# Performance work log

Hardware: AMD Instinct MI355X
Metric: run time of the kernel (lower is better)

Reference implementation:

```python
import jax, jax.numpy as jnp
import numpy as np

B, N, C, H = 4, 2048, 1024, 16
D = C // H  # head_dim = 64

def setup_inputs() -> dict:
    key = jax.random.key(0)
    k1, k2, k3, k4, k5, k6 = jax.random.split(key, 6)
    x = jax.random.normal(k1, (B, N, C), dtype=jnp.float32)
    rope_cos = jax.random.uniform(k2, (N, D), dtype=jnp.float32)
    rope_sin = jax.random.uniform(k3, (N, D), dtype=jnp.float32)
    w_qkv = jax.random.normal(k4, (3 * C, C), dtype=jnp.float32) * (C ** -0.5)
    w_proj = jax.random.normal(k5, (C, C), dtype=jnp.float32) * (C ** -0.5)
    b_proj = jax.random.normal(k6, (C,), dtype=jnp.float32) * 0.01
    return {"x": x, "rope_cos": rope_cos, "rope_sin": rope_sin,
            "w_qkv": w_qkv, "w_proj": w_proj, "b_proj": b_proj}

def _rotate_half(x):
    x1, x2 = jnp.split(x, 2, axis=-1)
    return jnp.concatenate((-x2, x1), axis=-1)

def _apply_rope(x, cos, sin):
    # x: [B,H,N,D]; cos/sin: [N,D] broadcast over B,H
    return x * cos + _rotate_half(x) * sin

def reference(x, rope_cos, rope_sin, w_qkv, w_proj, b_proj):
    Bc, Nc, Cc = x.shape
    scale = D ** -0.5
    qkv = jnp.einsum('bnc,fc->bnf', x, w_qkv)            # [B,N,3C]
    qkv = qkv.reshape(Bc, Nc, 3, H, D).transpose(2, 0, 3, 1, 4)  # [3,B,H,N,D]
    q, k, v = qkv[0], qkv[1], qkv[2]
    q = _apply_rope(q, rope_cos, rope_sin)
    k = _apply_rope(k, rope_cos, rope_sin)
    attn = jnp.einsum('bhnd,bhmd->bhnm', q, k) * scale   # [B,H,N,N]
    attn = jax.nn.softmax(attn, axis=-1)
    out = jnp.einsum('bhnm,bhmd->bhnd', attn, v)         # [B,H,N,D]
    out = out.transpose(0, 2, 1, 3).reshape(Bc, Nc, Cc)  # [B,N,C]
    return jnp.einsum('bnc,fc->bnf', out, w_proj) + b_proj
```

## Files before the change

kernel.cpp:

```cpp
#include <hip/hip_runtime.h>

#define MM   8192
#define CC   1024
#define F3   3072
#define NN   2048
#define HH   16
#define DD   64
#define QSCALE 0.1803368801111731f

typedef __attribute__((ext_vector_type(8))) __bf16 bf16x8;
typedef __attribute__((ext_vector_type(4))) float floatx4;
typedef __attribute__((ext_vector_type(4))) unsigned uintx4;

__device__ __forceinline__ unsigned short f2b(float f) {
  union { float f; unsigned int u; } v; v.f = f;
  unsigned int r = v.u + 0x7fffu + ((v.u >> 16) & 1u);
  return (unsigned short)(r >> 16);
}
__device__ __forceinline__ float b2f(unsigned short b) {
  union { unsigned int u; float f; } v; v.u = ((unsigned int)b) << 16;
  return v.f;
}

__device__ __forceinline__ void gl_lds16(const unsigned short* g, unsigned short* l) {
  __builtin_amdgcn_global_load_lds((const __attribute__((address_space(1))) void*)g,
                                   (__attribute__((address_space(3))) void*)l, 16, 0, 0);
}

__global__ __launch_bounds__(256) void cvt_all_k(const float* __restrict__ x,
                                                 const float* __restrict__ wqkv,
                                                 const float* __restrict__ wproj,
                                                 unsigned short* __restrict__ xb,
                                                 unsigned short* __restrict__ wqkvb,
                                                 unsigned short* __restrict__ wprojb) {
  const int N0 = MM * CC / 4, N1 = F3 * CC / 4, N2 = CC * CC / 4;
  const int total = N0 + N1 + N2;
  const int stride = (int)gridDim.x * 256;
  for (int i = blockIdx.x * 256 + threadIdx.x; i < total; i += stride) {
    const float* src;
    unsigned short* dst;
    int j;
    if (i < N0)            { src = x;     dst = xb;     j = i; }
    else if (i < N0 + N1)  { src = wqkv;  dst = wqkvb;  j = i - N0; }
    else                   { src = wproj; dst = wprojb; j = i - N0 - N1; }
    float4 v = ((const float4*)src)[j];
    ushort4 o;
    o.x = f2b(v.x); o.y = f2b(v.y); o.z = f2b(v.z); o.w = f2b(v.w);
    ((ushort4*)dst)[j] = o;
  }
}

template <int F, bool BF16OUT, bool ROPE>
__global__ __launch_bounds__(512, 2) void gemm_p(const unsigned short* __restrict__ A,
                                                 const unsigned short* __restrict__ Bm,
                                                 void* __restrict__ Cout,
                                                 const float* __restrict__ bias,
                                                 const float* __restrict__ rcp,
                                                 const float* __restrict__ spp, int K) {
  __shared__ alignas(16) unsigned short lA[3][128 * 64];
  __shared__ alignas(16) unsigned short lB[3][256 * 64];
  const int tid = threadIdx.x, lane = tid & 63, wave = tid >> 6;
  const int r16 = lane & 15, q4 = lane >> 4;
  const int wm = wave & 1, wn = wave >> 1;

  const int id = blockIdx.x;
  const int xcd = id & 7, slot = id >> 3;
  const int rx = xcd * 8 + (slot & 7), cy = slot >> 3;
  const int rowBase = rx * 128, colBase = cy * 256;

  const int cA0 = tid, cA1 = tid + 512;
  const int cB0 = tid, cB1 = tid + 512, cB2 = tid + 1024, cB3 = tid + 1536;
#define CHOFF(base, c) ((size_t)((base) + ((c) >> 3)) * K + ((((c) & 7) ^ (((c) >> 3) & 7)) << 3))
  const size_t aoff0 = CHOFF(rowBase, cA0), aoff1 = CHOFF(rowBase, cA1);
  const size_t boff0 = CHOFF(colBase, cB0), boff1 = CHOFF(colBase, cB1);
  const size_t boff2 = CHOFF(colBase, cB2), boff3 = CHOFF(colBase, cB3);
#undef CHOFF

#define STAGEP(kt, bsel) do { const int _k0 = (kt) * 64; \
    gl_lds16(A + aoff0 + _k0, &lA[bsel][cA0 * 8]); \
    gl_lds16(A + aoff1 + _k0, &lA[bsel][cA1 * 8]); \
    gl_lds16(Bm + boff0 + _k0, &lB[bsel][cB0 * 8]); \
    gl_lds16(Bm + boff1 + _k0, &lB[bsel][cB1 * 8]); \
    gl_lds16(Bm + boff2 + _k0, &lB[bsel][cB2 * 8]); \
    gl_lds16(Bm + boff3 + _k0, &lB[bsel][cB3 * 8]); } while (0)

  floatx4 acc[4][4];
  const floatx4 z = {0.f, 0.f, 0.f, 0.f};
#pragma unroll
  for (int i = 0; i < 4; ++i)
#pragma unroll
    for (int j = 0; j < 4; ++j) acc[i][j] = z;

  const int nt = K / 64;

  STAGEP(0, 0);
  STAGEP(1, 1);
  STAGEP(2, 2);
  asm volatile("s_waitcnt vmcnt(12)" ::: "memory");
  __builtin_amdgcn_s_barrier();
  __builtin_amdgcn_sched_barrier(0);

  int bs = 0;
  for (int t = 0; t < nt; ++t) {
    const unsigned short* la = &lA[bs][0];
    const unsigned short* lb = &lB[bs][0];
    bf16x8 af[4][2], bv[4][2];
#pragma unroll
    for (int im = 0; im < 4; ++im) {
      int row = wm * 64 + im * 16 + r16, r7 = row & 7;
      af[im][0] = *(const bf16x8*)(la + row * 64 + ((q4 ^ r7) << 3));
      af[im][1] = *(const bf16x8*)(la + row * 64 + (((4 + q4) ^ r7) << 3));
    }
#pragma unroll
    for (int jf = 0; jf < 4; ++jf) {
      int row = wn * 64 + jf * 16 + r16, r7 = row & 7;
      bv[jf][0] = *(const bf16x8*)(lb + row * 64 + ((q4 ^ r7) << 3));
      bv[jf][1] = *(const bf16x8*)(lb + row * 64 + (((4 + q4) ^ r7) << 3));
    }
    __builtin_amdgcn_s_setprio(1);
#pragma unroll
    for (int jf = 0; jf < 4; ++jf)
#pragma unroll
      for (int im = 0; im < 4; ++im) {
        acc[im][jf] = __builtin_amdgcn_mfma_f32_16x16x32_bf16(af[im][0], bv[jf][0], acc[im][jf], 0, 0, 0);
        acc[im][jf] = __builtin_amdgcn_mfma_f32_16x16x32_bf16(af[im][1], bv[jf][1], acc[im][jf], 0, 0, 0);
      }
    __builtin_amdgcn_s_setprio(0);

    __builtin_amdgcn_s_barrier();
    __builtin_amdgcn_sched_barrier(0);
    if (t + 3 < nt) {
      STAGEP(t + 3, bs);
      asm volatile("s_waitcnt vmcnt(12)" ::: "memory");
    } else {
      asm volatile("s_waitcnt vmcnt(0)" ::: "memory");
    }
    __builtin_amdgcn_sched_barrier(0);
    __builtin_amdgcn_s_barrier();
    __builtin_amdgcn_sched_barrier(0);
    bs = (bs == 2) ? 0 : bs + 1;
  }
#undef STAGEP

  if (ROPE) {
    int head = (colBase >> 6) + wn;
    if (head < 32) {
      const bool isq = head < 16;
#pragma unroll
      for (int im = 0; im < 4; ++im)
#pragma unroll
        for (int jf = 0; jf < 2; ++jf)
#pragma unroll
          for (int r = 0; r < 4; ++r) {
            int grow = rowBase + wm * 64 + im * 16 + q4 * 4 + r;
            int n = grow & (NN - 1);
            int dp = jf * 16 + r16;
            float x0 = acc[im][jf][r], x1 = acc[im][jf + 2][r];
            float c0 = rcp[n * DD + dp],      s0v = spp[n * DD + dp];
            float c1 = rcp[n * DD + dp + 32], s1v = spp[n * DD + dp + 32];
            float y0 = x0 * c0 - x1 * s0v;
            float y1 = x1 * c1 + x0 * s1v;
            if (isq) { y0 *= QSCALE; y1 *= QSCALE; }
            acc[im][jf][r] = y0;
            acc[im][jf + 2][r] = y1;
          }
    }
  }

#pragma unroll
  for (int im = 0; im < 4; ++im)
#pragma unroll
    for (int jf = 0; jf < 4; ++jf)
#pragma unroll
      for (int r = 0; r < 4; ++r) {
        int grow = rowBase + wm * 64 + im * 16 + q4 * 4 + r;
        int gcol = colBase + wn * 64 + jf * 16 + r16;
        if (BF16OUT)
          ((unsigned short*)Cout)[(size_t)grow * F + gcol] = f2b(acc[im][jf][r]);
        else
          ((float*)Cout)[(size_t)grow * F + gcol] = acc[im][jf][r] + bias[gcol];
      }
}

__global__ __launch_bounds__(256, 2) void attn_k(const unsigned short* __restrict__ qkv,
                                                 unsigned short* __restrict__ obuf) {
  __shared__ alignas(16) unsigned short sK[2][64 * 64];
  __shared__ alignas(16) unsigned short sVT[2][64 * 64];

  const int tid = threadIdx.x, lane = tid & 63, wave = tid >> 6;
  const int r16 = lane & 15, q4 = lane >> 4;

  const int id = blockIdx.x;
  const int xcd = id & 7, slot = id >> 3;
  const int bh = xcd * 8 + (slot >> 3);
  const int q0 = (slot & 7) * 256;
  const int b = bh >> 4, h = bh & 15;
  const unsigned short* qbase = qkv + (size_t)(b * NN) * F3 + h * DD;

  bf16x8 qf[4][2];
#pragma unroll
  for (int im = 0; im < 4; ++im)
#pragma unroll
    for (int kk = 0; kk < 2; ++kk)
      qf[im][kk] = *(const bf16x8*)(qbase +
          (size_t)(q0 + wave * 64 + im * 16 + r16) * F3 + kk * 32 + q4 * 8);

  const floatx4 z = {0.f, 0.f, 0.f, 0.f};
  floatx4 o[4][4];
  float lacc[4] = {0.f, 0.f, 0.f, 0.f};
#pragma unroll
  for (int im = 0; im < 4; ++im)
    for (int jd = 0; jd < 4; ++jd) o[im][jd] = z;

  const int krow0 = tid >> 3, kc8 = tid & 7;
  const int vkvp = tid >> 3, vc8 = tid & 7;
  const int mp = (vkvp & 16) | ((vkvp & 4) << 1) | ((vkvp & 2) << 1) |
                 ((vkvp & 8) >> 2) | (vkvp & 1);

  const int skoff0 = krow0 * 64 + ((kc8 ^ (krow0 & 7)) << 3);
  const int skoff1 = (krow0 + 32) * 64 + ((kc8 ^ ((krow0 + 32) & 7)) << 3);

  int4 kreg0 = *(const int4*)(qbase + (size_t)krow0 * F3 + CC + kc8 * 8);
  int4 kreg1 = *(const int4*)(qbase + (size_t)(krow0 + 32) * F3 + CC + kc8 * 8);
  int4 vreg0 = *(const int4*)(qbase + (size_t)(2 * vkvp) * F3 + 2 * CC + vc8 * 8);
  int4 vreg1 = *(const int4*)(qbase + (size_t)(2 * vkvp + 1) * F3 + 2 * CC + vc8 * 8);

  {
    *(int4*)(&sK[0][skoff0]) = kreg0;
    *(int4*)(&sK[0][skoff1]) = kreg1;
    const unsigned* a0 = (const unsigned*)&vreg0;
    const unsigned* a1 = (const unsigned*)&vreg1;
#pragma unroll
    for (int w = 0; w < 4; ++w) {
      unsigned lo = __builtin_amdgcn_perm(a1[w], a0[w], 0x05040100u);
      unsigned hi = __builtin_amdgcn_perm(a1[w], a0[w], 0x07060302u);
      int d0 = vc8 * 8 + 2 * w;
      int sw0 = (2 * w + vc8) & 7;
      int sw1 = (2 * w + 1 + vc8) & 7;
      *(unsigned*)(&sVT[0][d0 * 64 + (((mp >> 2) ^ sw0) << 3) + 2 * (mp & 3)]) = lo;
      *(unsigned*)(&sVT[0][(d0 + 1) * 64 + (((mp >> 2) ^ sw1) << 3) + 2 * (mp & 3)]) = hi;
    }
  }
  {
    const unsigned short* nb = qbase + (size_t)64 * F3;
    kreg0 = *(const int4*)(nb + (size_t)krow0 * F3 + CC + kc8 * 8);
    kreg1 = *(const int4*)(nb + (size_t)(krow0 + 32) * F3 + CC + kc8 * 8);
    vreg0 = *(const int4*)(nb + (size_t)(2 * vkvp) * F3 + 2 * CC + vc8 * 8);
    vreg1 = *(const int4*)(nb + (size_t)(2 * vkvp + 1) * F3 + 2 * CC + vc8 * 8);
  }
  __syncthreads();

  for (int t = 0; t < NN / 64; ++t) {
    const int p = t & 1;

    if (t + 1 < NN / 64) {
      *(int4*)(&sK[p ^ 1][skoff0]) = kreg0;
      *(int4*)(&sK[p ^ 1][skoff1]) = kreg1;
      const unsigned* a0 = (const unsigned*)&vreg0;
      const unsigned* a1 = (const unsigned*)&vreg1;
#pragma unroll
      for (int w = 0; w < 4; ++w) {
        unsigned lo = __builtin_amdgcn_perm(a1[w], a0[w], 0x05040100u);
        unsigned hi = __builtin_amdgcn_perm(a1[w], a0[w], 0x07060302u);
        int d0 = vc8 * 8 + 2 * w;
        int sw0 = (2 * w + vc8) & 7;
        int sw1 = (2 * w + 1 + vc8) & 7;
        *(unsigned*)(&sVT[p ^ 1][d0 * 64 + (((mp >> 2) ^ sw0) << 3) + 2 * (mp & 3)]) = lo;
        *(unsigned*)(&sVT[p ^ 1][(d0 + 1) * 64 + (((mp >> 2) ^ sw1) << 3) + 2 * (mp & 3)]) = hi;
      }
      if (t + 2 < NN / 64) {
        const unsigned short* nb = qbase + (size_t)((t + 2) * 64) * F3;
        kreg0 = *(const int4*)(nb + (size_t)krow0 * F3 + CC + kc8 * 8);
        kreg1 = *(const int4*)(nb + (size_t)(krow0 + 32) * F3 + CC + kc8 * 8);
        vreg0 = *(const int4*)(nb + (size_t)(2 * vkvp) * F3 + 2 * CC + vc8 * 8);
        vreg1 = *(const int4*)(nb + (size_t)(2 * vkvp + 1) * F3 + 2 * CC + vc8 * 8);
      }
    }

    floatx4 s[4][4];
    __builtin_amdgcn_s_setprio(1);
#pragma unroll
    for (int jn = 0; jn < 4; ++jn) {
      int row = jn * 16 + r16;
      bf16x8 kf0 = *(const bf16x8*)(&sK[p][row * 64 + ((q4 ^ (row & 7)) << 3)]);
      bf16x8 kf1 = *(const bf16x8*)(&sK[p][row * 64 + (((4 + q4) ^ (row & 7)) << 3)]);
#pragma unroll
      for (int im = 0; im < 4; ++im) {
        floatx4 a = z;
        a = __builtin_amdgcn_mfma_f32_16x16x32_bf16(kf0, qf[im][0], a, 0, 0, 0);
        a = __builtin_amdgcn_mfma_f32_16x16x32_bf16(kf1, qf[im][1], a, 0, 0, 0);
        s[im][jn] = a;
      }
    }
    __builtin_amdgcn_s_setprio(0);

    bf16x8 pf[4][2];
#pragma unroll
    for (int im = 0; im < 4; ++im) {
#pragma unroll
      for (int kk = 0; kk < 2; ++kk) {
        uintx4 pk;
#pragma unroll
        for (int j2 = 0; j2 < 2; ++j2) {
          int jn = 2 * kk + j2;
          float p0 = __builtin_amdgcn_exp2f(s[im][jn][0]);
          float p1 = __builtin_amdgcn_exp2f(s[im][jn][1]);
          float p2 = __builtin_amdgcn_exp2f(s[im][jn][2]);
          float p3 = __builtin_amdgcn_exp2f(s[im][jn][3]);
          lacc[im] += (p0 + p1) + (p2 + p3);
          asm("v_cvt_pk_bf16_f32 %0, %1, %2" : "=v"(pk[2 * j2]) : "v"(p0), "v"(p1));
          asm("v_cvt_pk_bf16_f32 %0, %1, %2" : "=v"(pk[2 * j2 + 1]) : "v"(p2), "v"(p3));
        }
        pf[im][kk] = __builtin_bit_cast(bf16x8, pk);
      }
    }

    __builtin_amdgcn_s_setprio(1);
#pragma unroll
    for (int jd = 0; jd < 4; ++jd) {
      int d = jd * 16 + r16;
      int swr = (d + (d >> 3)) & 7;
      bf16x8 vf0 = *(const bf16x8*)(&sVT[p][d * 64 + ((q4 ^ swr) << 3)]);
      bf16x8 vf1 = *(const bf16x8*)(&sVT[p][d * 64 + (((4 + q4) ^ swr) << 3)]);
#pragma unroll
      for (int im = 0; im < 4; ++im) {
        o[im][jd] = __builtin_amdgcn_mfma_f32_16x16x32_bf16(pf[im][0], vf0, o[im][jd], 0, 0, 0);
        o[im][jd] = __builtin_amdgcn_mfma_f32_16x16x32_bf16(pf[im][1], vf1, o[im][jd], 0, 0, 0);
      }
    }
    __builtin_amdgcn_s_setprio(0);

    __syncthreads();
  }

#pragma unroll
  for (int im = 0; im < 4; ++im) {
    float l = lacc[im];
    l += __shfl_xor(l, 16);
    l += __shfl_xor(l, 32);
    float inv = 1.0f / l;
#pragma unroll
    for (int r = 0; r < 4; ++r) {
      float invr = __shfl(inv, q4 * 4 + r);
      int row = q0 + wave * 64 + im * 16 + q4 * 4 + r;
#pragma unroll
      for (int jd = 0; jd < 4; ++jd) {
        int col = h * DD + jd * 16 + r16;
        obuf[(size_t)(b * NN + row) * CC + col] = f2b(o[im][jd][r] * invr);
      }
    }
  }
}

extern "C" void kernel_launch(void* const* d_in, const int* in_sizes, int n_in,
                              void* d_out, int out_size, void* d_ws, size_t ws_size,
                              hipStream_t stream) {
  const float* x     = (const float*)d_in[0];
  const float* rc    = (const float*)d_in[1];
  const float* rs    = (const float*)d_in[2];
  const float* wqkv  = (const float*)d_in[3];
  const float* wproj = (const float*)d_in[4];
  const float* bproj = (const float*)d_in[5];
  float* out = (float*)d_out;

  char* w = (char*)d_ws;
  unsigned short* xb     = (unsigned short*)(w);
  unsigned short* wqkvb  = (unsigned short*)(w + 16777216);
  unsigned short* wprojb = (unsigned short*)(w + 23068672);
  unsigned short* qkvb   = (unsigned short*)(w + 25165824);
  unsigned short* obuf   = (unsigned short*)(w + 75497472);

  cvt_all_k<<<2048, 256, 0, stream>>>(x, wqkv, wproj, xb, wqkvb, wprojb);

  gemm_p<F3, true, true><<<768, 512, 0, stream>>>(
      xb, wqkvb, qkvb, nullptr, rc, rs, CC);

  attn_k<<<512, 256, 0, stream>>>(qkvb, obuf);

  gemm_p<CC, false, false><<<256, 512, 0, stream>>>(
      obuf, wprojb, out, bproj, nullptr, nullptr, CC);
}
```

Measured before the change: 264.2 us.

## Add 128x128-tile direct-to-LDS projection GEMM and load attention K via global-to-LDS

The output projection moves from the 512-thread gemm_p to a new 256-thread gemm_d2 kernel. It uses 128x128 tiles, so 512 blocks are launched, and double-buffers A/B through direct global-to-LDS loads with XOR-swizzled source addresses. In the attention kernel, K tiles are now fetched with global-to-LDS loads instead of passing through registers, which frees VGPRs and removes the ds_write work. V still goes through registers for its transpose. The risks are that the attention loop may not wait correctly on the async LDS loads before its barrier, and that the smaller projection tiles need more global traffic.

```diff
diff --git a/kernel.cpp b/kernel.cpp
--- a/kernel.cpp
+++ b/kernel.cpp
@@ -182,6 +182,109 @@
       }
 }
 
+template <int F>
+__global__ __launch_bounds__(256, 2) void gemm_d2(const unsigned short* __restrict__ A,
+                                                  const unsigned short* __restrict__ Bm,
+                                                  float* __restrict__ Cout,
+                                                  const float* __restrict__ bias, int K) {
+  __shared__ alignas(16) unsigned short lA[2][128 * 64];
+  __shared__ alignas(16) unsigned short lB[2][128 * 64];
+  const int tid = threadIdx.x, lane = tid & 63, wave = tid >> 6;
+  const int r16 = lane & 15, q4 = lane >> 4;
+  const int wm = wave & 1, wn = wave >> 1;
+
+  const int id = blockIdx.x;
+  const int xcd = id & 7, slot = id >> 3;
+  const int rx = xcd * 8 + (slot & 7), cy = slot >> 3;
+  const int rowBase = rx * 128, colBase = cy * 128;
+
+#define CHOFF(base, c) ((size_t)((base) + ((c) >> 3)) * K + ((((c) & 7) ^ (((c) >> 3) & 7)) << 3))
+  size_t aoff[4], boff[4];
+#pragma unroll
+  for (int i = 0; i < 4; ++i) {
+    aoff[i] = CHOFF(rowBase, tid + i * 256);
+    boff[i] = CHOFF(colBase, tid + i * 256);
+  }
+#undef CHOFF
+
+#define STAGED(kt, bsel) do { const int _k0 = (kt) * 64; \
+    gl_lds16(A + aoff[0] + _k0, &lA[bsel][(tid) * 8]); \
+    gl_lds16(A + aoff[1] + _k0, &lA[bsel][(tid + 256) * 8]); \
+    gl_lds16(A + aoff[2] + _k0, &lA[bsel][(tid + 512) * 8]); \
+    gl_lds16(A + aoff[3] + _k0, &lA[bsel][(tid + 768) * 8]); \
+    gl_lds16(Bm + boff[0] + _k0, &lB[bsel][(tid) * 8]); \
+    gl_lds16(Bm + boff[1] + _k0, &lB[bsel][(tid + 256) * 8]); \
+    gl_lds16(Bm + boff[2] + _k0, &lB[bsel][(tid + 512) * 8]); \
+    gl_lds16(Bm + boff[3] + _k0, &lB[bsel][(tid + 768) * 8]); } while (0)
+
+  floatx4 acc[4][4];
+  const floatx4 z = {0.f, 0.f, 0.f, 0.f};
+#pragma unroll
+  for (int i = 0; i < 4; ++i)
+#pragma unroll
+    for (int j = 0; j < 4; ++j) acc[i][j] = z;
+
+  const int nt = K / 64;
+
+  STAGED(0, 0);
+  STAGED(1, 1);
+  asm volatile("s_waitcnt vmcnt(8)" ::: "memory");
+  __builtin_amdgcn_s_barrier();
+  __builtin_amdgcn_sched_barrier(0);
+
+  for (int t = 0; t < nt; ++t) {
+    const int bs = t & 1;
+    const unsigned short* la = &lA[bs][0];
+    const unsigned short* lb = &lB[bs][0];
+    bf16x8 af[4][2], bv[4][2];
+#pragma unroll
+    for (int im = 0; im < 4; ++im) {
+      int row = wm * 64 + im * 16 + r16, r7 = row & 7;
+      af[im][0] = *(const bf16x8*)(la + row * 64 + ((q4 ^ r7) << 3));
+      af[im][1] = *(const bf16x8*)(la + row * 64 + (((4 + q4) ^ r7) << 3));
+    }
+#pragma unroll
+    for (int jf = 0; jf < 4; ++jf) {
+      int row = wn * 64 + jf * 16 + r16, r7 = row & 7;
+      bv[jf][0] = *(const bf16x8*)(lb + row * 64 + ((q4 ^ r7) << 3));
+      bv[jf][1] = *(const bf16x8*)(lb + row * 64 + (((4 + q4) ^ r7) << 3));
+    }
+    __builtin_amdgcn_s_setprio(1);
+#pragma unroll
+    for (int jf = 0; jf < 4; ++jf)
+#pragma unroll
+      for (int im = 0; im < 4; ++im) {
+        acc[im][jf] = __builtin_amdgcn_mfma_f32_16x16x32_bf16(af[im][0], bv[jf][0], acc[im][jf], 0, 0, 0);
+        acc[im][jf] = __builtin_amdgcn_mfma_f32_16x16x32_bf16(af[im][1], bv[jf][1], acc[im][jf], 0, 0, 0);
+      }
+    __builtin_amdgcn_s_setprio(0);
+
+    __builtin_amdgcn_s_barrier();
+    __builtin_amdgcn_sched_barrier(0);
+    if (t + 2 < nt) {
+      STAGED(t + 2, bs);
+      asm volatile("s_waitcnt vmcnt(8)" ::: "memory");
+    } else {
+      asm volatile("s_waitcnt vmcnt(0)" ::: "memory");
+    }
+    __builtin_amdgcn_sched_barrier(0);
+    __builtin_amdgcn_s_barrier();
+    __builtin_amdgcn_sched_barrier(0);
+  }
+#undef STAGED
+
+#pragma unroll
+  for (int im = 0; im < 4; ++im)
+#pragma unroll
+    for (int jf = 0; jf < 4; ++jf)
+#pragma unroll
+      for (int r = 0; r < 4; ++r) {
+        int grow = rowBase + wm * 64 + im * 16 + q4 * 4 + r;
+        int gcol = colBase + wn * 64 + jf * 16 + r16;
+        Cout[(size_t)grow * F + gcol] = acc[im][jf][r] + bias[gcol];
+      }
+}
+
 __global__ __launch_bounds__(256, 2) void attn_k(const unsigned short* __restrict__ qkv,
                                                  unsigned short* __restrict__ obuf) {
   __shared__ alignas(16) unsigned short sK[2][64 * 64];
@@ -212,22 +315,19 @@
   for (int im = 0; im < 4; ++im)
     for (int jd = 0; jd < 4; ++jd) o[im][jd] = z;
 
-  const int krow0 = tid >> 3, kc8 = tid & 7;
+  const int kr0 = tid >> 3, kr1 = kr0 + 32;
+  const size_t ksrc0 = (size_t)kr0 * F3 + CC + (((tid & 7) ^ (kr0 & 7)) << 3);
+  const size_t ksrc1 = (size_t)kr1 * F3 + CC + (((tid & 7) ^ (kr1 & 7)) << 3);
   const int vkvp = tid >> 3, vc8 = tid & 7;
   const int mp = (vkvp & 16) | ((vkvp & 4) << 1) | ((vkvp & 2) << 1) |
                  ((vkvp & 8) >> 2) | (vkvp & 1);
 
-  const int skoff0 = krow0 * 64 + ((kc8 ^ (krow0 & 7)) << 3);
-  const int skoff1 = (krow0 + 32) * 64 + ((kc8 ^ ((krow0 + 32) & 7)) << 3);
-
-  int4 kreg0 = *(const int4*)(qbase + (size_t)krow0 * F3 + CC + kc8 * 8);
-  int4 kreg1 = *(const int4*)(qbase + (size_t)(krow0 + 32) * F3 + CC + kc8 * 8);
   int4 vreg0 = *(const int4*)(qbase + (size_t)(2 * vkvp) * F3 + 2 * CC + vc8 * 8);
   int4 vreg1 = *(const int4*)(qbase + (size_t)(2 * vkvp + 1) * F3 + 2 * CC + vc8 * 8);
+  gl_lds16(qbase + ksrc0, &sK[0][tid * 8]);
+  gl_lds16(qbase + ksrc1, &sK[0][(tid + 256) * 8]);
 
   {
-    *(int4*)(&sK[0][skoff0]) = kreg0;
-    *(int4*)(&sK[0][skoff1]) = kreg1;
     const unsigned* a0 = (const unsigned*)&vreg0;
     const unsigned* a1 = (const unsigned*)&vreg1;
 #pragma unroll
@@ -243,8 +343,6 @@
   }
   {
     const unsigned short* nb = qbase + (size_t)64 * F3;
-    kreg0 = *(const int4*)(nb + (size_t)krow0 * F3 + CC + kc8 * 8);
-    kreg1 = *(const int4*)(nb + (size_t)(krow0 + 32) * F3 + CC + kc8 * 8);
     vreg0 = *(const int4*)(nb + (size_t)(2 * vkvp) * F3 + 2 * CC + vc8 * 8);
     vreg1 = *(const int4*)(nb + (size_t)(2 * vkvp + 1) * F3 + 2 * CC + vc8 * 8);
   }
@@ -254,8 +352,9 @@
     const int p = t & 1;
 
     if (t + 1 < NN / 64) {
-      *(int4*)(&sK[p ^ 1][skoff0]) = kreg0;
-      *(int4*)(&sK[p ^ 1][skoff1]) = kreg1;
+      const unsigned short* nb = qbase + (size_t)((t + 1) * 64) * F3;
+      gl_lds16(nb + ksrc0, &sK[p ^ 1][tid * 8]);
+      gl_lds16(nb + ksrc1, &sK[p ^ 1][(tid + 256) * 8]);
       const unsigned* a0 = (const unsigned*)&vreg0;
       const unsigned* a1 = (const unsigned*)&vreg1;
 #pragma unroll
@@ -269,11 +368,9 @@
         *(unsigned*)(&sVT[p ^ 1][(d0 + 1) * 64 + (((mp >> 2) ^ sw1) << 3) + 2 * (mp & 3)]) = hi;
       }
       if (t + 2 < NN / 64) {
-        const unsigned short* nb = qbase + (size_t)((t + 2) * 64) * F3;
-        kreg0 = *(const int4*)(nb + (size_t)krow0 * F3 + CC + kc8 * 8);
-        kreg1 = *(const int4*)(nb + (size_t)(krow0 + 32) * F3 + CC + kc8 * 8);
-        vreg0 = *(const int4*)(nb + (size_t)(2 * vkvp) * F3 + 2 * CC + vc8 * 8);
-        vreg1 = *(const int4*)(nb + (size_t)(2 * vkvp + 1) * F3 + 2 * CC + vc8 * 8);
+        const unsigned short* nb2 = qbase + (size_t)((t + 2) * 64) * F3;
+        vreg0 = *(const int4*)(nb2 + (size_t)(2 * vkvp) * F3 + 2 * CC + vc8 * 8);
+        vreg1 = *(const int4*)(nb2 + (size_t)(2 * vkvp + 1) * F3 + 2 * CC + vc8 * 8);
       }
     }
 
@@ -377,6 +474,5 @@
 
   attn_k<<<512, 256, 0, stream>>>(qkvb, obuf);
 
-  gemm_p<CC, false, false><<<256, 512, 0, stream>>>(
-      obuf, wprojb, out, bproj, nullptr, nullptr, CC);
-}
+  gemm_d2<CC><<<512, 256, 0, stream>>>(obuf, wprojb, out, bproj, CC);
+}
```

Result: no change. 265.4 us (+0.4%).
